# Performance work log

Measured on AMD Instinct MI355X. Metric: run time of the kernel, lower is better.

## Reference

```python
import jax, jax.numpy as jnp
import numpy as np

D = 500  # hidden width hard-coded in the module

def _lrelu(x):
    # nn.LeakyReLU default negative_slope = 0.01
    return jnp.where(x > 0, x, 0.01 * x)

def setup_inputs() -> dict:
    key = jax.random.key(0)
    ks = jax.random.split(key, 20)
    T, B = 2048, 64
    inp = {
        "pitches": jax.random.normal(ks[0], (T, B, 128), dtype=jnp.float32),
        "velocities": jax.random.normal(ks[1], (T, B, 128), dtype=jnp.float32),
        "durations": jax.random.uniform(ks[2], (T, B, 1), dtype=jnp.float32),
        "steps": jax.random.uniform(ks[3], (T, B, 1), dtype=jnp.float32),
        # learned params (torch Linear convention: W is [out, in])
        "Wp": jax.random.normal(ks[4], (D, 128), dtype=jnp.float32) * 0.05,
        "bp": jax.random.normal(ks[5], (D,), dtype=jnp.float32) * 0.05,
        "Wv": jax.random.normal(ks[6], (D, 128), dtype=jnp.float32) * 0.05,
        "bv": jax.random.normal(ks[7], (D,), dtype=jnp.float32) * 0.05,
        "Wd": jax.random.normal(ks[8], (D, 1), dtype=jnp.float32) * 0.05,
        "bd": jax.random.normal(ks[9], (D,), dtype=jnp.float32) * 0.05,
        "Ws": jax.random.normal(ks[10], (D, 1), dtype=jnp.float32) * 0.05,
        "bs": jax.random.normal(ks[11], (D,), dtype=jnp.float32) * 0.05,
        "W1": jax.random.normal(ks[12], (D, D), dtype=jnp.float32) * 0.05,
        "b1": jax.random.normal(ks[13], (D,), dtype=jnp.float32) * 0.05,
        "W2": jax.random.normal(ks[14], (D, D), dtype=jnp.float32) * 0.05,
        "b2": jax.random.normal(ks[15], (D,), dtype=jnp.float32) * 0.05,
        "Wi": jax.random.normal(ks[16], (D, D), dtype=jnp.float32) * 0.05,
        "bi": jax.random.normal(ks[17], (D,), dtype=jnp.float32) * 0.05,
        "W3": jax.random.normal(ks[18], (1, D), dtype=jnp.float32) * 0.05,
        "b3": jax.random.normal(ks[19], (1,), dtype=jnp.float32) * 0.05,
    }
    return inp

def reference(pitches, velocities, durations, steps,
              Wp, bp, Wv, bv, Wd, bd, Ws, bs,
              W1, b1, W2, b2, Wi, bi, W3, b3):
    # Note: in the original torch code the LSTMCell output is computed then
    # discarded (overwritten), and `info` at step t depends only on inputs at
    # step t. Thus the final output depends only on the last timestep through
    # the embed-sum -> LeakyReLU MLP -> linear_intermediate chain.
    # Vectorized over all T timesteps (same per-step math as the loop body).
    add = (jnp.einsum('tbi,oi->tbo', pitches, Wp) + bp
           + jnp.einsum('tbi,oi->tbo', velocities, Wv) + bv
           + jnp.einsum('tbi,oi->tbo', durations, Wd) + bd
           + jnp.einsum('tbi,oi->tbo', steps, Ws) + bs)      # [T,B,500]
    h = _lrelu(jnp.einsum('tbi,oi->tbo', add, W1) + b1)
    h = _lrelu(jnp.einsum('tbi,oi->tbo', h, W2) + b2)
    info = jnp.einsum('tbi,oi->tbo', h, Wi) + bi              # [T,B,500]
    out = jax.nn.sigmoid(info[-1] @ W3.T + b3)                # [B,1]
    return out
```

## Files before the change

kernel.cpp:

```cpp
#include <hip/hip_runtime.h>

#define DD 500
#define BB 64
#define TT 2048
#define KP 128
#define VCHUNKS 32
#define VPSTRIDE 512

__global__ __launch_bounds__(256) void k_embed_v(
    const float* __restrict__ pitches, const float* __restrict__ velocities,
    const float* __restrict__ durations, const float* __restrict__ steps,
    const float* __restrict__ Wp, const float* __restrict__ bp,
    const float* __restrict__ Wv, const float* __restrict__ bv,
    const float* __restrict__ Wd, const float* __restrict__ bd,
    const float* __restrict__ Wst, const float* __restrict__ bs,
    const float* __restrict__ Wi, const float* __restrict__ W3,
    float* __restrict__ addT, float* __restrict__ vpart)
{
    const int tid = threadIdx.x;
    const int bid = blockIdx.x;

    if (bid >= 125) {
        const int oc = bid - 125;
        const int obeg = oc * 16;
        const int k0 = tid;
        const int k1 = tid + 256;
        float acc0 = 0.f, acc1 = 0.f;
        #pragma unroll
        for (int i = 0; i < 16; ++i) {
            const int o = obeg + i;
            const int oc_ = o < DD ? o : DD - 1;
            const float w = o < DD ? W3[oc_] : 0.f;
            acc0 += w * Wi[(size_t)oc_ * DD + k0];
            if (k1 < DD) acc1 += w * Wi[(size_t)oc_ * DD + k1];
        }
        vpart[oc * VPSTRIDE + k0] = acc0;
        if (k1 < DD) vpart[oc * VPSTRIDE + k1] = acc1;
        return;
    }

    __shared__ float lds[KP * BB];
    const int b = tid & 63;
    const int o = __builtin_amdgcn_readfirstlane(bid * 4 + (tid >> 6));
    const float* __restrict__ wp = Wp + o * KP;
    const float* __restrict__ wv = Wv + o * KP;

    float a0 = 0.f, a1 = 0.f, a2 = 0.f, a3 = 0.f;

    const float4* Psrc = (const float4*)(pitches + (size_t)(TT - 1) * BB * KP);
    const float4* Vsrc = (const float4*)(velocities + (size_t)(TT - 1) * BB * KP);

    for (int j = tid; j < BB * KP / 4; j += 256) {
        float4 p = Psrc[j];
        int pb = j >> 5;
        int k0 = (j & 31) * 4;
        lds[(k0 + 0) * BB + ((pb + k0 + 0) & 63)] = p.x;
        lds[(k0 + 1) * BB + ((pb + k0 + 1) & 63)] = p.y;
        lds[(k0 + 2) * BB + ((pb + k0 + 2) & 63)] = p.z;
        lds[(k0 + 3) * BB + ((pb + k0 + 3) & 63)] = p.w;
    }
    __syncthreads();
    for (int k = 0; k < KP; k += 4) {
        a0 += lds[(k + 0) * BB + ((b + k + 0) & 63)] * wp[k + 0];
        a1 += lds[(k + 1) * BB + ((b + k + 1) & 63)] * wp[k + 1];
        a2 += lds[(k + 2) * BB + ((b + k + 2) & 63)] * wp[k + 2];
        a3 += lds[(k + 3) * BB + ((b + k + 3) & 63)] * wp[k + 3];
    }
    __syncthreads();

    for (int j = tid; j < BB * KP / 4; j += 256) {
        float4 p = Vsrc[j];
        int pb = j >> 5;
        int k0 = (j & 31) * 4;
        lds[(k0 + 0) * BB + ((pb + k0 + 0) & 63)] = p.x;
        lds[(k0 + 1) * BB + ((pb + k0 + 1) & 63)] = p.y;
        lds[(k0 + 2) * BB + ((pb + k0 + 2) & 63)] = p.z;
        lds[(k0 + 3) * BB + ((pb + k0 + 3) & 63)] = p.w;
    }
    __syncthreads();
    for (int k = 0; k < KP; k += 4) {
        a0 += lds[(k + 0) * BB + ((b + k + 0) & 63)] * wv[k + 0];
        a1 += lds[(k + 1) * BB + ((b + k + 1) & 63)] * wv[k + 1];
        a2 += lds[(k + 2) * BB + ((b + k + 2) & 63)] * wv[k + 2];
        a3 += lds[(k + 3) * BB + ((b + k + 3) & 63)] * wv[k + 3];
    }

    const float dur = durations[(size_t)(TT - 1) * BB + b];
    const float st  = steps[(size_t)(TT - 1) * BB + b];
    const float acc = bp[o] + bv[o] + bd[o] + bs[o]
                    + dur * Wd[o] + st * Wst[o]
                    + (a0 + a1) + (a2 + a3);
    addT[o * BB + b] = acc;
}

__global__ __launch_bounds__(256) void k_dense(
    const float* __restrict__ Ain, const float* __restrict__ W,
    const float* __restrict__ bias, float* __restrict__ Aout, int leaky)
{
    const int tid = threadIdx.x;
    const int b = tid & 63;
    const int o = __builtin_amdgcn_readfirstlane(blockIdx.x * 4 + (tid >> 6));
    const float* __restrict__ wrow = W + o * DD;

    float a0 = 0.f, a1 = 0.f, a2 = 0.f, a3 = 0.f;
    float a4 = 0.f, a5 = 0.f, a6 = 0.f, a7 = 0.f;
    for (int k = 0; k < 496; k += 8) {
        a0 += Ain[(k + 0) * BB + b] * wrow[k + 0];
        a1 += Ain[(k + 1) * BB + b] * wrow[k + 1];
        a2 += Ain[(k + 2) * BB + b] * wrow[k + 2];
        a3 += Ain[(k + 3) * BB + b] * wrow[k + 3];
        a4 += Ain[(k + 4) * BB + b] * wrow[k + 4];
        a5 += Ain[(k + 5) * BB + b] * wrow[k + 5];
        a6 += Ain[(k + 6) * BB + b] * wrow[k + 6];
        a7 += Ain[(k + 7) * BB + b] * wrow[k + 7];
    }
    a0 += Ain[496 * BB + b] * wrow[496];
    a1 += Ain[497 * BB + b] * wrow[497];
    a2 += Ain[498 * BB + b] * wrow[498];
    a3 += Ain[499 * BB + b] * wrow[499];

    float acc = bias[o] + ((a0 + a1) + (a2 + a3)) + ((a4 + a5) + (a6 + a7));
    if (leaky) acc = acc > 0.f ? acc : 0.01f * acc;
    Aout[o * BB + b] = acc;
}

__global__ __launch_bounds__(256) void k_out(
    const float* __restrict__ h2T, const float* __restrict__ vpart,
    const float* __restrict__ W3, const float* __restrict__ bi,
    const float* __restrict__ b3, float* __restrict__ out)
{
    __shared__ float vv[DD];
    __shared__ float partial[4][BB];
    const int tid = threadIdx.x;

    for (int k = tid; k < DD; k += 256) {
        float s0 = 0.f, s1 = 0.f, s2 = 0.f, s3 = 0.f;
        #pragma unroll
        for (int oc = 0; oc < VCHUNKS; oc += 4) {
            s0 += vpart[(oc + 0) * VPSTRIDE + k];
            s1 += vpart[(oc + 1) * VPSTRIDE + k];
            s2 += vpart[(oc + 2) * VPSTRIDE + k];
            s3 += vpart[(oc + 3) * VPSTRIDE + k];
        }
        vv[k] = (s0 + s1) + (s2 + s3);
    }
    __syncthreads();

    const int b = tid & 63;
    const int w = tid >> 6;
    const int kbeg = w * 125;

    float accA = 0.f, accB = 0.f;
    for (int k = kbeg; k < kbeg + 125; ++k) {
        accA += h2T[k * BB + b] * vv[k];
        accB += W3[k] * bi[k];
    }
    partial[w][b] = accA + accB;
    __syncthreads();
    if (w == 0) {
        float s = partial[0][b] + partial[1][b] + partial[2][b] + partial[3][b]
                + b3[0];
        out[b] = 1.f / (1.f + __expf(-s));
    }
}

extern "C" void kernel_launch(void* const* d_in, const int* in_sizes, int n_in,
                              void* d_out, int out_size, void* d_ws, size_t ws_size,
                              hipStream_t stream)
{
    const float* pitches    = (const float*)d_in[0];
    const float* velocities = (const float*)d_in[1];
    const float* durations  = (const float*)d_in[2];
    const float* steps      = (const float*)d_in[3];
    const float* Wp  = (const float*)d_in[4];
    const float* bp  = (const float*)d_in[5];
    const float* Wv  = (const float*)d_in[6];
    const float* bv  = (const float*)d_in[7];
    const float* Wd  = (const float*)d_in[8];
    const float* bd  = (const float*)d_in[9];
    const float* Wst = (const float*)d_in[10];
    const float* bs  = (const float*)d_in[11];
    const float* W1  = (const float*)d_in[12];
    const float* b1  = (const float*)d_in[13];
    const float* W2  = (const float*)d_in[14];
    const float* b2  = (const float*)d_in[15];
    const float* Wi  = (const float*)d_in[16];
    const float* bi  = (const float*)d_in[17];
    const float* W3  = (const float*)d_in[18];
    const float* b3  = (const float*)d_in[19];

    float* ws    = (float*)d_ws;
    float* addT  = ws;
    float* h1T   = ws + 32000;
    float* h2T   = ws + 64000;
    float* vpart = ws + 96000;

    float* out = (float*)d_out;

    k_embed_v<<<125 + VCHUNKS, 256, 0, stream>>>(pitches, velocities, durations,
                                                 steps, Wp, bp, Wv, bv, Wd, bd,
                                                 Wst, bs, Wi, W3, addT, vpart);
    k_dense<<<125, 256, 0, stream>>>(addT, W1, b1, h1T, 1);
    k_dense<<<125, 256, 0, stream>>>(h1T, W2, b2, h2T, 1);
    k_out<<<1, 256, 0, stream>>>(h2T, vpart, W3, bi, b3, out);
}
```

Before: 212.0 us.

## Split dense k-range across waves, prefetch W1/W2 into cache during embed

```diff
diff --git a/kernel.cpp b/kernel.cpp
--- a/kernel.cpp
+++ b/kernel.cpp
@@ -15,10 +15,27 @@
     const float* __restrict__ Wd, const float* __restrict__ bd,
     const float* __restrict__ Wst, const float* __restrict__ bs,
     const float* __restrict__ Wi, const float* __restrict__ W3,
-    float* __restrict__ addT, float* __restrict__ vpart)
+    const float* __restrict__ W1, const float* __restrict__ W2,
+    float* __restrict__ addT, float* __restrict__ vpart,
+    float* __restrict__ dummy)
 {
     const int tid = threadIdx.x;
     const int bid = blockIdx.x;
+
+    if (bid >= 157) {
+        const int pb = bid - 157;
+        const int slice = pb >> 3;
+        const float4* W1f = (const float4*)W1;
+        const float4* W2f = (const float4*)W2;
+        float acc = 0.f;
+        const int jend = (slice + 1) * 15625;
+        for (int j = slice * 15625 + tid; j < jend; j += 256) {
+            float4 p = (j < 62500) ? W1f[j] : W2f[j - 62500];
+            acc += p.x + p.y + p.z + p.w;
+        }
+        dummy[bid] = acc;
+        return;
+    }
 
     if (bid >= 125) {
         const int oc = bid - 125;
@@ -97,14 +114,18 @@
     const float* __restrict__ Ain, const float* __restrict__ W,
     const float* __restrict__ bias, float* __restrict__ Aout, int leaky)
 {
+    __shared__ float partial[4][BB];
     const int tid = threadIdx.x;
     const int b = tid & 63;
-    const int o = __builtin_amdgcn_readfirstlane(blockIdx.x * 4 + (tid >> 6));
+    const int w = tid >> 6;
+    const int o = blockIdx.x;
     const float* __restrict__ wrow = W + o * DD;
+    const int kbeg = w * 125;
 
     float a0 = 0.f, a1 = 0.f, a2 = 0.f, a3 = 0.f;
     float a4 = 0.f, a5 = 0.f, a6 = 0.f, a7 = 0.f;
-    for (int k = 0; k < 496; k += 8) {
+    #pragma unroll 3
+    for (int k = kbeg; k < kbeg + 120; k += 8) {
         a0 += Ain[(k + 0) * BB + b] * wrow[k + 0];
         a1 += Ain[(k + 1) * BB + b] * wrow[k + 1];
         a2 += Ain[(k + 2) * BB + b] * wrow[k + 2];
@@ -114,14 +135,22 @@
         a6 += Ain[(k + 6) * BB + b] * wrow[k + 6];
         a7 += Ain[(k + 7) * BB + b] * wrow[k + 7];
     }
-    a0 += Ain[496 * BB + b] * wrow[496];
-    a1 += Ain[497 * BB + b] * wrow[497];
-    a2 += Ain[498 * BB + b] * wrow[498];
-    a3 += Ain[499 * BB + b] * wrow[499];
-
-    float acc = bias[o] + ((a0 + a1) + (a2 + a3)) + ((a4 + a5) + (a6 + a7));
-    if (leaky) acc = acc > 0.f ? acc : 0.01f * acc;
-    Aout[o * BB + b] = acc;
+    {
+        const int k = kbeg + 120;
+        a0 += Ain[(k + 0) * BB + b] * wrow[k + 0];
+        a1 += Ain[(k + 1) * BB + b] * wrow[k + 1];
+        a2 += Ain[(k + 2) * BB + b] * wrow[k + 2];
+        a3 += Ain[(k + 3) * BB + b] * wrow[k + 3];
+        a4 += Ain[(k + 4) * BB + b] * wrow[k + 4];
+    }
+    partial[w][b] = ((a0 + a1) + (a2 + a3)) + ((a4 + a5) + (a6 + a7));
+    __syncthreads();
+    if (w == 0) {
+        float acc = bias[o] + (partial[0][b] + partial[1][b])
+                            + (partial[2][b] + partial[3][b]);
+        if (leaky) acc = acc > 0.f ? acc : 0.01f * acc;
+        Aout[o * BB + b] = acc;
+    }
 }
 
 __global__ __launch_bounds__(256) void k_out(
@@ -135,14 +164,19 @@
 
     for (int k = tid; k < DD; k += 256) {
         float s0 = 0.f, s1 = 0.f, s2 = 0.f, s3 = 0.f;
+        float s4 = 0.f, s5 = 0.f, s6 = 0.f, s7 = 0.f;
         #pragma unroll
-        for (int oc = 0; oc < VCHUNKS; oc += 4) {
+        for (int oc = 0; oc < VCHUNKS; oc += 8) {
             s0 += vpart[(oc + 0) * VPSTRIDE + k];
             s1 += vpart[(oc + 1) * VPSTRIDE + k];
             s2 += vpart[(oc + 2) * VPSTRIDE + k];
             s3 += vpart[(oc + 3) * VPSTRIDE + k];
+            s4 += vpart[(oc + 4) * VPSTRIDE + k];
+            s5 += vpart[(oc + 5) * VPSTRIDE + k];
+            s6 += vpart[(oc + 6) * VPSTRIDE + k];
+            s7 += vpart[(oc + 7) * VPSTRIDE + k];
         }
-        vv[k] = (s0 + s1) + (s2 + s3);
+        vv[k] = ((s0 + s1) + (s2 + s3)) + ((s4 + s5) + (s6 + s7));
     }
     __syncthreads();
 
@@ -194,13 +228,14 @@
     float* h1T   = ws + 32000;
     float* h2T   = ws + 64000;
     float* vpart = ws + 96000;
+    float* dummy = ws + 96000 + VCHUNKS * VPSTRIDE;
 
     float* out = (float*)d_out;
 
-    k_embed_v<<<125 + VCHUNKS, 256, 0, stream>>>(pitches, velocities, durations,
-                                                 steps, Wp, bp, Wv, bv, Wd, bd,
-                                                 Wst, bs, Wi, W3, addT, vpart);
-    k_dense<<<125, 256, 0, stream>>>(addT, W1, b1, h1T, 1);
-    k_dense<<<125, 256, 0, stream>>>(h1T, W2, b2, h2T, 1);
+    k_embed_v<<<221, 256, 0, stream>>>(pitches, velocities, durations, steps,
+                                       Wp, bp, Wv, bv, Wd, bd, Wst, bs,
+                                       Wi, W3, W1, W2, addT, vpart, dummy);
+    k_dense<<<500, 256, 0, stream>>>(addT, W1, b1, h1T, 1);
+    k_dense<<<500, 256, 0, stream>>>(h1T, W2, b2, h2T, 1);
     k_out<<<1, 256, 0, stream>>>(h2T, vpart, W3, bi, b3, out);
 }
```

Measured after the change: 220.6 us. 4.1% more time.
